# Optimization experiments

Measured on AMD Instinct MI355X. Metric: run time of the kernel, lower is better.

## Reference

```python
import jax, jax.numpy as jnp
import numpy as np

M = 12          # persons per frame
K = 2           # partition channels from conv1da (1024 = 2*512)
D = 512         # GCN channel dim / LSTM hidden
C_IN = 4096     # backbone feature dim
NUM_CLASSES = 8


def setup_inputs() -> dict:
    key = jax.random.key(0)
    ks = jax.random.split(key, 8)
    N, T = 16, 32
    NT = N * T
    base_out = jax.random.normal(ks[0], (NT, M, C_IN), dtype=jnp.float32)
    dist = jax.random.uniform(ks[1], (N, T, 3, K, M, M), dtype=jnp.float32)
    # conv1da: Conv1d(4096 -> 1024, k=1, bias=False) == matmul with [1024, 4096]
    w_a = jax.random.normal(ks[2], (K * D, C_IN), dtype=jnp.float32) * 0.02
    # LSTM(512, 512, 1): torch gate order i, f, g, o
    s = 1.0 / np.sqrt(D)
    w_ih = jax.random.uniform(ks[3], (4 * D, D), minval=-s, maxval=s, dtype=jnp.float32)
    w_hh = jax.random.uniform(ks[4], (4 * D, D), minval=-s, maxval=s, dtype=jnp.float32)
    b_ih = jax.random.uniform(ks[5], (4 * D,), minval=-s, maxval=s, dtype=jnp.float32)
    b_hh = jax.random.uniform(ks[6], (4 * D,), minval=-s, maxval=s, dtype=jnp.float32)
    # gclassifier: Linear(512 -> num_classes)
    w_cls = jax.random.normal(ks[7], (NUM_CLASSES, D), dtype=jnp.float32) * 0.01
    b_cls = jnp.zeros((NUM_CLASSES,), dtype=jnp.float32)
    return {"base_out": base_out, "dist": dist, "w_a": w_a,
            "w_ih": w_ih, "w_hh": w_hh, "b_ih": b_ih, "b_hh": b_hh,
            "w_cls": w_cls, "b_cls": b_cls, "n_videos": N}


def reference(base_out, dist, w_a, w_ih, w_hh, b_ih, b_hh, w_cls, b_cls, n_videos):
    NT = base_out.shape[0]
    N = n_videos
    T = NT // N
    # conv1da (1x1 conv, no bias): [NT, M, 4096] -> [NT, K*D, M] -> [NT, K, D, M]
    node1 = jnp.einsum('nmc,oc->nom', base_out, w_a).reshape(NT, K, D, M)
    # fused three-way adjacency aggregation: node1a + node1b + node1c
    A = (dist[:, :, 2] + dist[:, :, 1] + dist[:, :, 0]).reshape(NT, K, M, M)
    node = jnp.einsum('nkcv,nkvw->ncw', node1, A)  # [NT, D, M]
    node = jax.nn.relu(node)
    # AdaptiveAvgPool1d(1) over the M persons
    pooled = node.mean(axis=2)                      # [NT, D]
    seq = pooled.reshape(N, T, D)
    # torch nn.LSTM default batch_first=False: iterates over axis 0 (N), batch=T
    def step(carry, x_t):
        h, c = carry
        g = x_t @ w_ih.T + b_ih + h @ w_hh.T + b_hh  # [T, 4D]
        i, f, gg, o = jnp.split(g, 4, axis=-1)
        c = jax.nn.sigmoid(f) * c + jax.nn.sigmoid(i) * jnp.tanh(gg)
        h = jax.nn.sigmoid(o) * jnp.tanh(c)
        return (h, c), h
    h0 = jnp.zeros((T, D), dtype=seq.dtype)
    c0 = jnp.zeros((T, D), dtype=seq.dtype)
    _, hs = jax.lax.scan(step, (h0, c0), seq)       # [N, T, D]
    last = hs[:, -1, :]                              # video_feat[:, -1, :]
    return last @ w_cls.T + b_cls                    # [N, num_classes]
```

## Files before the change

### kernel.cpp

```cpp
#include <hip/hip_runtime.h>
#include <math.h>

#define MM 12
#define KK 2
#define DD 512
#define CIN 4096
#define NCLS 8
#define NV 16
#define TT 32

typedef unsigned long long u64;
typedef __attribute__((ext_vector_type(8))) __bf16 bf16x8;
typedef __attribute__((ext_vector_type(4))) float f32x4;

#define PART_F   0
#define POOLED_F 786432
#define TAGGX_F  794752
#define HGLOB_F  796800
#define GX_F     813184
#define PART_KS_STRIDE (192 * 1024)

#define MFMA_BF16(A, B, C) __builtin_amdgcn_mfma_f32_16x16x32_bf16((A), (B), (C), 0, 0, 0)
#define LOADR(p)      __hip_atomic_load((p), __ATOMIC_RELAXED, __HIP_MEMORY_SCOPE_AGENT)
#define LOADACQ(p)    __hip_atomic_load((p), __ATOMIC_ACQUIRE, __HIP_MEMORY_SCOPE_AGENT)
#define STOREREL(p, v) __hip_atomic_store((p), (v), __ATOMIC_RELEASE, __HIP_MEMORY_SCOPE_AGENT)
#define LOADS(p)      __hip_atomic_load((p), __ATOMIC_RELAXED, __HIP_MEMORY_SCOPE_SYSTEM)
#define EXCHS(p, v)   (void)__hip_atomic_exchange((p), (v), __ATOMIC_RELAXED, __HIP_MEMORY_SCOPE_SYSTEM)

static __device__ __forceinline__ u64 ld_sc0(const u64* p) {
  u64 v;
  asm volatile("global_load_dwordx2 %0, %1, off sc0\n\ts_waitcnt vmcnt(0)"
               : "=v"(v) : "v"(p) : "memory");
  return v;
}
static __device__ __forceinline__ void st_sc0(u64* p, u64 v) {
  asm volatile("global_store_dwordx2 %0, %1, off sc0" :: "v"(p), "v"(v) : "memory");
}

static __device__ __forceinline__ void cvt_store(
    unsigned short* __restrict__ hb, unsigned short* __restrict__ lb,
    int idx, float4 v) {
  unsigned ux = __float_as_uint(v.x), uy = __float_as_uint(v.y);
  unsigned uz = __float_as_uint(v.z), uw = __float_as_uint(v.w);
  *(uint2*)&hb[idx] = make_uint2((ux >> 16) | (uy & 0xFFFF0000u),
                                 (uz >> 16) | (uw & 0xFFFF0000u));
  unsigned lx = __float_as_uint(v.x - __uint_as_float(ux & 0xFFFF0000u));
  unsigned ly = __float_as_uint(v.y - __uint_as_float(uy & 0xFFFF0000u));
  unsigned lz = __float_as_uint(v.z - __uint_as_float(uz & 0xFFFF0000u));
  unsigned lw = __float_as_uint(v.w - __uint_as_float(uw & 0xFFFF0000u));
  *(uint2*)&lb[idx] = make_uint2((lx >> 16) | (ly & 0xFFFF0000u),
                                 (lz >> 16) | (lw & 0xFFFF0000u));
}

__global__ __launch_bounds__(64, 1) void k_gemm(
    const float* __restrict__ base_out, const float* __restrict__ w_a,
    float* __restrict__ part)
{
  const int wg = blockIdx.x;
  const int ks = wg & 3;
  const int ot = (wg >> 2) & 63;
  const int jq = (wg >> 8) & 3;
  const int cc0 = ks * 1024;
  const int lane = threadIdx.x;

  __shared__ __align__(16) unsigned short Ah[16 * 40], Al[16 * 40];
  __shared__ __align__(16) unsigned short Bh[48 * 40], Bl[48 * 40];

  const int sq = lane & 7;
  const int sr = lane >> 3;

  unsigned boff[6];
#pragma unroll
  for (int rep = 0; rep < 6; ++rep) {
    const int jl = sr + 8 * rep;
    const int j = jq * 48 + jl;
    const int n = j / 12, m = j - n * 12;
    boff[rep] = (unsigned)(((n * TT + 31) * MM + m) * CIN + cc0 + sq * 4);
  }
  unsigned aoff[2];
#pragma unroll
  for (int repA = 0; repA < 2; ++repA)
    aoff[repA] = (unsigned)((ot * 16 + sr + 8 * repA) * CIN + cc0 + sq * 4);

  f32x4 acc0 = {0.f, 0.f, 0.f, 0.f}, acc1 = acc0, acc2 = acc0;

  float4 pa0[2], pb0[6], pa1[2], pb1[6];
#pragma unroll
  for (int repA = 0; repA < 2; ++repA) pa0[repA] = *(const float4*)&w_a[aoff[repA]];
#pragma unroll
  for (int rep = 0; rep < 6; ++rep) pb0[rep] = *(const float4*)&base_out[boff[rep]];
#pragma unroll
  for (int repA = 0; repA < 2; ++repA) {
    aoff[repA] += 32; pa1[repA] = *(const float4*)&w_a[aoff[repA]];
  }
#pragma unroll
  for (int rep = 0; rep < 6; ++rep) {
    boff[rep] += 32; pb1[rep] = *(const float4*)&base_out[boff[rep]];
  }

#define STAGE_SET(PA, PB)                                                   \
  {                                                                         \
    _Pragma("unroll")                                                       \
    for (int repA = 0; repA < 2; ++repA)                                    \
      cvt_store(Ah, Al, (sr + 8 * repA) * 40 + sq * 4, PA[repA]);           \
    _Pragma("unroll")                                                       \
    for (int rep = 0; rep < 6; ++rep)                                       \
      cvt_store(Bh, Bl, (sr + 8 * rep) * 40 + sq * 4, PB[rep]);             \
  }
#define LOAD_SET(PA, PB)                                                    \
  {                                                                         \
    _Pragma("unroll")                                                       \
    for (int repA = 0; repA < 2; ++repA) {                                  \
      aoff[repA] += 32; PA[repA] = *(const float4*)&w_a[aoff[repA]];        \
    }                                                                       \
    _Pragma("unroll")                                                       \
    for (int rep = 0; rep < 6; ++rep) {                                     \
      boff[rep] += 32; PB[rep] = *(const float4*)&base_out[boff[rep]];      \
    }                                                                       \
  }
#define MFMA_STEP()                                                         \
  {                                                                         \
    const int koff = (lane >> 4) * 8;                                       \
    const int fra = (lane & 15) * 40 + koff;                                \
    bf16x8 oh = *(const bf16x8*)&Ah[fra];                                   \
    bf16x8 ol = *(const bf16x8*)&Al[fra];                                   \
    {                                                                       \
      const int r0 = (0 * 16 + (lane & 15)) * 40 + koff;                    \
      bf16x8 jh = *(const bf16x8*)&Bh[r0], jl = *(const bf16x8*)&Bl[r0];    \
      acc0 = MFMA_BF16(jh, oh, acc0);                                       \
      acc0 = MFMA_BF16(jh, ol, acc0);                                       \
      acc0 = MFMA_BF16(jl, oh, acc0);                                       \
    }                                                                       \
    {                                                                       \
      const int r1 = (1 * 16 + (lane & 15)) * 40 + koff;                    \
      bf16x8 jh = *(const bf16x8*)&Bh[r1], jl = *(const bf16x8*)&Bl[r1];    \
      acc1 = MFMA_BF16(jh, oh, acc1);                                       \
      acc1 = MFMA_BF16(jh, ol, acc1);                                       \
      acc1 = MFMA_BF16(jl, oh, acc1);                                       \
    }                                                                       \
    {                                                                       \
      const int r2 = (2 * 16 + (lane & 15)) * 40 + koff;                    \
      bf16x8 jh = *(const bf16x8*)&Bh[r2], jl = *(const bf16x8*)&Bl[r2];    \
      acc2 = MFMA_BF16(jh, oh, acc2);                                       \
      acc2 = MFMA_BF16(jh, ol, acc2);                                       \
      acc2 = MFMA_BF16(jl, oh, acc2);                                       \
    }                                                                       \
  }

  for (int st = 0; st < 32; st += 2) {
    STAGE_SET(pa0, pb0);
    if (st + 2 < 32) LOAD_SET(pa0, pb0);
    MFMA_STEP();
    STAGE_SET(pa1, pb1);
    if (st + 3 < 32) LOAD_SET(pa1, pb1);
    MFMA_STEP();
  }
#undef STAGE_SET
#undef LOAD_SET
#undef MFMA_STEP

  const int o = ot * 16 + (lane & 15);
  const int jr = (lane >> 4) * 4;
#pragma unroll
  for (int r = 0; r < 4; ++r) {
    part[((size_t)ks * 192 + jq * 48 + 0 * 16 + jr + r) * 1024 + o] = acc0[r];
    part[((size_t)ks * 192 + jq * 48 + 1 * 16 + jr + r) * 1024 + o] = acc1[r];
    part[((size_t)ks * 192 + jq * 48 + 2 * 16 + jr + r) * 1024 + o] = acc2[r];
  }
}

__global__ __launch_bounds__(256, 1) void k_pool(
    const float* __restrict__ dist, const float* __restrict__ part,
    float* __restrict__ pooled)
{
  const int wg = blockIdx.x;
  const int tid = threadIdx.x;

  __shared__ float Asum_s[KK * MM * MM];

  const int n = wg >> 4, cb = (wg & 15) * 32;
  const unsigned dbase = (unsigned)((n * TT + 31) * (3 * KK * MM * MM));
  for (int f = tid; f < KK * MM * MM; f += 256)
    Asum_s[f] = dist[dbase + f] + dist[dbase + KK * MM * MM + f]
              + dist[dbase + 2 * KK * MM * MM + f];
  __syncthreads();
  if (tid < 32) {
    const int c = cb + tid;
    float nd[KK][MM];
#pragma unroll
    for (int k = 0; k < KK; ++k)
#pragma unroll
      for (int v = 0; v < MM; ++v) {
        const size_t off = (size_t)(n * MM + v) * 1024 + k * DD + c;
        nd[k][v] = part[off] + part[off + PART_KS_STRIDE]
                 + part[off + 2 * PART_KS_STRIDE] + part[off + 3 * PART_KS_STRIDE];
      }
    float accm = 0.f;
#pragma unroll
    for (int w = 0; w < MM; ++w) {
      float sw = 0.f;
#pragma unroll
      for (int k = 0; k < KK; ++k)
#pragma unroll
        for (int v = 0; v < MM; ++v) sw += nd[k][v] * Asum_s[(k * MM + v) * MM + w];
      accm += fmaxf(sw, 0.f);
    }
    pooled[n * DD + c] = accm * (1.f / 12.f);
  }
}

__global__ __launch_bounds__(1024, 1) void k_rest(
    const float* __restrict__ pooled,
    const float* __restrict__ w_ih, const float* __restrict__ w_hh,
    const float* __restrict__ b_ih, const float* __restrict__ b_hh,
    const float* __restrict__ w_cls, const float* __restrict__ b_cls,
    unsigned* __restrict__ tagGX, float* __restrict__ gxg,
    u64* __restrict__ hg64, float* __restrict__ out)
{
  const int wg = blockIdx.x;
  const int tid = threadIdx.x;

  __shared__ __align__(16) float whh_s[64][516];
  __shared__ float gx_s[16][64];
  __shared__ __align__(16) float h_s[DD];
  __shared__ float dot_s[64];

  if ((wg & 7) != 0) {
    const int k = wg & 7;
    if (k > 4) return;
    const int m = wg >> 3;
    const int dd = m + 32 * (k - 1);
    if (tid < 256) {
      const int n = tid & 15, j = tid >> 4;
      const int gr = dd * 16 + j;
      const float4* wr = (const float4*)&w_ih[(size_t)gr * DD];
      const float4* pv = (const float4*)&pooled[(size_t)n * DD];
      float a = 0.f;
#pragma unroll 8
      for (int q = 0; q < DD / 4; ++q) {
        float4 x = wr[q], y = pv[q];
        a += x.x * y.x + x.y * y.y + x.z * y.z + x.w * y.w;
      }
      gxg[m * 1024 + n * 64 + (k - 1) * 16 + j] = a + b_ih[gr] + b_hh[gr];
    }
    __syncthreads();
    if (tid == 0) STOREREL(&tagGX[dd * 16], 1u);
    return;
  }

  const int w = wg >> 3;

  for (int f = tid; f < 64 * 128; f += 1024) {
    const int rr = f >> 7, c4 = (f & 127) * 4;
    const int grow = (rr >> 4) * DD + w * 16 + (rr & 15);
    *(float4*)&whh_s[rr][c4] = *(const float4*)&w_hh[(size_t)grow * DD + c4];
  }
  if (tid < 64) {
    bool done;
    do {
      int t0 = (int)LOADR(&tagGX[(w + 32 * (tid & 3)) * 16]);
      done = __all(t0 == 1);
    } while (!done);
  }
  __syncthreads();
  gx_s[tid >> 6][tid & 63] =
      __uint_as_float(LOADS((const unsigned*)&gxg[w * 1024 + tid]));
  __syncthreads();

  {
    float c_reg = 0.f;
    const int r = tid >> 4;
    const int lj = tid & 15;

    for (int s = 0; s < NV; ++s) {
      if (s == 0) {
        if (tid < DD) h_s[tid] = 0.f;
      } else {
        if (tid < DD) {
          const u64* p = &hg64[(size_t)(s - 1) * DD + tid];
          u64 v = ld_sc0(p);
          while ((unsigned)v != (unsigned)s) {
            v = LOADS(p);
            if ((unsigned)v == (unsigned)s) break;
            v = ld_sc0(p);
          }
          h_s[tid] = __uint_as_float((unsigned)(v >> 32));
        }
      }
      __syncthreads();

      float p = 0.f;
      const float4* wrow = (const float4*)&whh_s[r][0];
      const float4* hv4 = (const float4*)h_s;
#pragma unroll
      for (int q = 0; q < 8; ++q) {
        float4 wv = wrow[lj + 16 * q];
        float4 hv = hv4[lj + 16 * q];
        p += wv.x * hv.x + wv.y * hv.y + wv.z * hv.z + wv.w * hv.w;
      }
#pragma unroll
      for (int off = 8; off; off >>= 1) p += __shfl_down(p, off, 16);
      if (lj == 0) dot_s[r] = p;
      __syncthreads();

      if (tid < 16) {
        const float pi = gx_s[s][tid]      + dot_s[tid];
        const float pf = gx_s[s][16 + tid] + dot_s[16 + tid];
        const float pg = gx_s[s][32 + tid] + dot_s[32 + tid];
        const float po = gx_s[s][48 + tid] + dot_s[48 + tid];
        const float si = 1.f / (1.f + expf(-pi));
        const float sf = 1.f / (1.f + expf(-pf));
        const float so = 1.f / (1.f + expf(-po));
        c_reg = sf * c_reg + si * tanhf(pg);
        const float hn = so * tanhf(c_reg);
        const u64 pk = ((u64)__float_as_uint(hn) << 32) | (u64)(unsigned)(s + 1);
        u64* pp = &hg64[(size_t)s * DD + w * 16 + tid];
        st_sc0(pp, pk);
        EXCHS(pp, pk);
      }
    }
  }

  if (wg == 0) {
    float* scratch = &whh_s[0][0];
    if (tid < DD) {
      u64 vv[NV];
#pragma unroll
      for (int n = 0; n < NV; ++n) vv[n] = LOADS(&hg64[(size_t)n * DD + tid]);
#pragma unroll
      for (int n = 0; n < NV; ++n) {
        u64 v = vv[n];
        while ((unsigned)v != (unsigned)(n + 1))
          v = LOADS(&hg64[(size_t)n * DD + tid]);
        scratch[n * 516 + tid] = __uint_as_float((unsigned)(v >> 32));
      }
    }
    __syncthreads();
    if (tid < NV * NCLS) {
      const int n = tid >> 3, cl = tid & 7;
      const float4* hv = (const float4*)&scratch[n * 516];
      const float4* wv = (const float4*)(w_cls + (size_t)cl * DD);
      float a = b_cls[cl];
#pragma unroll 8
      for (int q = 0; q < DD / 4; ++q) {
        float4 x = hv[q], y = wv[q];
        a += x.x * y.x + x.y * y.y + x.z * y.z + x.w * y.w;
      }
      out[tid] = a;
    }
  }
}

extern "C" void kernel_launch(void* const* d_in, const int* in_sizes, int n_in,
                              void* d_out, int out_size, void* d_ws, size_t ws_size,
                              hipStream_t stream) {
  const float* base_out = (const float*)d_in[0];
  const float* dist     = (const float*)d_in[1];
  const float* w_a      = (const float*)d_in[2];
  const float* w_ih     = (const float*)d_in[3];
  const float* w_hh     = (const float*)d_in[4];
  const float* b_ih     = (const float*)d_in[5];
  const float* b_hh     = (const float*)d_in[6];
  const float* w_cls    = (const float*)d_in[7];
  const float* b_cls    = (const float*)d_in[8];
  float* out = (float*)d_out;

  float* ws = (float*)d_ws;
  float* part   = ws + PART_F;
  float* pooled = ws + POOLED_F;
  unsigned* tagGX = (unsigned*)(ws + TAGGX_F);
  u64* hg64 = (u64*)(ws + HGLOB_F);
  float* gxg = ws + GX_F;

  k_gemm<<<dim3(1024), 64, 0, stream>>>(base_out, w_a, part);
  k_pool<<<dim3(256), 256, 0, stream>>>(dist, part, pooled);
  k_rest<<<dim3(256), 1024, 0, stream>>>(pooled, w_ih, w_hh, b_ih, b_hh,
                                         w_cls, b_cls, tagGX, gxg, hg64, out);
}
```

Baseline: 253.0 us.

## Split input-gate dot products across all threads and peel first LSTM step

The gate-projection blocks now split each 512-long dot product into four quarters across all 1024 threads and reduce the partials through shared memory, where before only 256 threads did the work. The recurrent blocks load their W_hh slice into registers before waiting on the gate tag. They then compute step 0 directly from the gates, since h0 is zero, and publish it before writing W_hh to shared memory. This overlaps the weight load with the wait and takes the first step off the serial recurrence chain, at the cost of extra registers and another shared buffer.

```diff
diff --git a/kernel.cpp b/kernel.cpp
--- a/kernel.cpp
+++ b/kernel.cpp
@@ -224,24 +224,35 @@
   __shared__ float gx_s[16][64];
   __shared__ __align__(16) float h_s[DD];
   __shared__ float dot_s[64];
+  __shared__ float gxp_s[1024];
 
   if ((wg & 7) != 0) {
     const int k = wg & 7;
     if (k > 4) return;
     const int m = wg >> 3;
     const int dd = m + 32 * (k - 1);
-    if (tid < 256) {
-      const int n = tid & 15, j = tid >> 4;
+    {
+      const int q4 = tid >> 8;
+      const int r = tid & 255;
+      const int n = r & 15, j = r >> 4;
       const int gr = dd * 16 + j;
       const float4* wr = (const float4*)&w_ih[(size_t)gr * DD];
       const float4* pv = (const float4*)&pooled[(size_t)n * DD];
       float a = 0.f;
 #pragma unroll 8
-      for (int q = 0; q < DD / 4; ++q) {
+      for (int q = q4 * 32; q < q4 * 32 + 32; ++q) {
         float4 x = wr[q], y = pv[q];
         a += x.x * y.x + x.y * y.y + x.z * y.z + x.w * y.w;
       }
-      gxg[m * 1024 + n * 64 + (k - 1) * 16 + j] = a + b_ih[gr] + b_hh[gr];
+      gxp_s[tid] = a;
+    }
+    __syncthreads();
+    if (tid < 256) {
+      const int n = tid & 15, j = tid >> 4;
+      const int gr = dd * 16 + j;
+      const float a = ((gxp_s[tid] + gxp_s[tid + 256]) + gxp_s[tid + 512])
+                    + gxp_s[tid + 768] + b_ih[gr] + b_hh[gr];
+      gxg[m * 1024 + n * 64 + (k - 1) * 16 + j] = a;
     }
     __syncthreads();
     if (tid == 0) STOREREL(&tagGX[dd * 16], 1u);
@@ -249,11 +260,15 @@
   }
 
   const int w = wg >> 3;
-
-  for (int f = tid; f < 64 * 128; f += 1024) {
+  float c_reg = 0.f;
+
+  float4 wtmp[8];
+#pragma unroll
+  for (int it = 0; it < 8; ++it) {
+    const int f = tid + it * 1024;
     const int rr = f >> 7, c4 = (f & 127) * 4;
     const int grow = (rr >> 4) * DD + w * 16 + (rr & 15);
-    *(float4*)&whh_s[rr][c4] = *(const float4*)&w_hh[(size_t)grow * DD + c4];
+    wtmp[it] = *(const float4*)&w_hh[(size_t)grow * DD + c4];
   }
   if (tid < 64) {
     bool done;
@@ -267,25 +282,44 @@
       __uint_as_float(LOADS((const unsigned*)&gxg[w * 1024 + tid]));
   __syncthreads();
 
+  if (tid < 16) {
+    const float pi = gx_s[0][tid]      + 0.0f;
+    const float pf = gx_s[0][16 + tid] + 0.0f;
+    const float pg = gx_s[0][32 + tid] + 0.0f;
+    const float po = gx_s[0][48 + tid] + 0.0f;
+    const float si = 1.f / (1.f + expf(-pi));
+    const float sf = 1.f / (1.f + expf(-pf));
+    const float so = 1.f / (1.f + expf(-po));
+    c_reg = sf * c_reg + si * tanhf(pg);
+    const float hn = so * tanhf(c_reg);
+    const u64 pk = ((u64)__float_as_uint(hn) << 32) | (u64)1u;
+    u64* pp = &hg64[w * 16 + tid];
+    st_sc0(pp, pk);
+    EXCHS(pp, pk);
+  }
+
+#pragma unroll
+  for (int it = 0; it < 8; ++it) {
+    const int f = tid + it * 1024;
+    const int rr = f >> 7, c4 = (f & 127) * 4;
+    *(float4*)&whh_s[rr][c4] = wtmp[it];
+  }
+  __syncthreads();
+
   {
-    float c_reg = 0.f;
     const int r = tid >> 4;
     const int lj = tid & 15;
 
-    for (int s = 0; s < NV; ++s) {
-      if (s == 0) {
-        if (tid < DD) h_s[tid] = 0.f;
-      } else {
-        if (tid < DD) {
-          const u64* p = &hg64[(size_t)(s - 1) * DD + tid];
-          u64 v = ld_sc0(p);
-          while ((unsigned)v != (unsigned)s) {
-            v = LOADS(p);
-            if ((unsigned)v == (unsigned)s) break;
-            v = ld_sc0(p);
-          }
-          h_s[tid] = __uint_as_float((unsigned)(v >> 32));
+    for (int s = 1; s < NV; ++s) {
+      if (tid < DD) {
+        const u64* p = &hg64[(size_t)(s - 1) * DD + tid];
+        u64 v = ld_sc0(p);
+        while ((unsigned)v != (unsigned)s) {
+          v = LOADS(p);
+          if ((unsigned)v == (unsigned)s) break;
+          v = ld_sc0(p);
         }
+        h_s[tid] = __uint_as_float((unsigned)(v >> 32));
       }
       __syncthreads();
 
```

Result: no change. 256.6 us (+1.4%).
